# Kernel optimization log

Hardware: AMD Instinct MI355X
Metric: run time of the kernel (lower is better)

Reference implementation:

```python
import jax, jax.numpy as jnp
import numpy as np

B, S, D = 4, 128, 4096
H, KV, HD = 32, 8, 128
REP = H // KV  # GQA repeat factor = 4


def setup_inputs() -> dict:
    key = jax.random.key(0)
    ks = jax.random.split(key, 10)
    scale = 0.02
    x = jax.random.normal(ks[0], (B, S, D), dtype=jnp.float32)
    # projection weights stored as (in, out) so y = x @ W + b (== torch Linear)
    wq = jax.random.normal(ks[1], (D, H * HD), dtype=jnp.float32) * scale
    bq = jax.random.normal(ks[2], (H * HD,), dtype=jnp.float32) * scale
    wk = jax.random.normal(ks[3], (D, KV * HD), dtype=jnp.float32) * scale
    bk = jax.random.normal(ks[4], (KV * HD,), dtype=jnp.float32) * scale
    wv = jax.random.normal(ks[5], (D, KV * HD), dtype=jnp.float32) * scale
    bv = jax.random.normal(ks[6], (KV * HD,), dtype=jnp.float32) * scale
    wo = jax.random.normal(ks[7], (H * HD, D), dtype=jnp.float32) * scale
    bo = jax.random.normal(ks[8], (D,), dtype=jnp.float32) * scale
    # rotary frequencies: theta=10000, half-dim = HD//2 = 64
    inv_freq = 1.0 / (10000.0 ** (jnp.arange(0, HD, 2, dtype=jnp.float32) / HD))
    t = jnp.arange(S, dtype=jnp.float32)
    angles = jnp.outer(t, inv_freq)  # (S, 64)
    freqs_cos = jnp.cos(angles)
    freqs_sin = jnp.sin(angles)
    # additive causal mask (S, S): 0 on/below diagonal, -inf above
    mask = jnp.where(jnp.tril(jnp.ones((S, S), dtype=bool)), 0.0, -jnp.inf).astype(jnp.float32)
    cache_k = jnp.zeros((B, S, KV, HD), dtype=jnp.float32)
    cache_v = jnp.zeros((B, S, KV, HD), dtype=jnp.float32)
    return {
        "x": x, "start_pos": 0, "freqs_cos": freqs_cos, "freqs_sin": freqs_sin,
        "mask": mask, "cache_k": cache_k, "cache_v": cache_v,
        "wq": wq, "bq": bq, "wk": wk, "bk": bk, "wv": wv, "bv": bv,
        "wo": wo, "bo": bo,
    }


def _rope(t, cos, sin):
    # t: (B, S, h, HD); treat last dim as HD//2 complex pairs (real, imag)
    tr = t.reshape(*t.shape[:-1], HD // 2, 2)
    tre, tim = tr[..., 0], tr[..., 1]
    c = cos[None, :, None, :]  # (1, S, 1, HD//2)
    s = sin[None, :, None, :]
    out_re = tre * c - tim * s
    out_im = tre * s + tim * c
    return jnp.stack([out_re, out_im], axis=-1).reshape(t.shape)


def reference(x, start_pos, freqs_cos, freqs_sin, mask, cache_k, cache_v,
              wq, bq, wk, bk, wv, bv, wo, bo):
    bsz, seq_len, _ = x.shape
    q = (x @ wq + bq).reshape(bsz, seq_len, H, HD)
    k = (x @ wk + bk).reshape(bsz, seq_len, KV, HD)
    v = (x @ wv + bv).reshape(bsz, seq_len, KV, HD)
    q = _rope(q, freqs_cos, freqs_sin)
    k = _rope(k, freqs_cos, freqs_sin)
    # KV-cache append (functional)
    cache_k = cache_k.at[:bsz, start_pos:start_pos + seq_len].set(k)
    cache_v = cache_v.at[:bsz, start_pos:start_pos + seq_len].set(v)
    keys = cache_k[:bsz, :start_pos + seq_len]    # (B, T, KV, HD)
    vals = cache_v[:bsz, :start_pos + seq_len]
    # GQA head expansion (repeat_interleave on head dim)
    keys = jnp.repeat(keys, REP, axis=2)          # (B, T, H, HD)
    vals = jnp.repeat(vals, REP, axis=2)
    scale = 1.0 / jnp.sqrt(jnp.float32(HD))
    scores = jnp.einsum('bqhd,bkhd->bhqk', q, keys) * scale + mask
    attn = jax.nn.softmax(scores, axis=-1)
    out = jnp.einsum('bhqk,bkhd->bqhd', attn, vals).reshape(bsz, seq_len, H * HD)
    return out @ wo + bo
```

## Files before the change

kernel.cpp:

```cpp
#include <hip/hip_runtime.h>
#include <math.h>


#define B_   4
#define S_   128
#define D_   4096
#define H_   32
#define KV_  8
#define HD_  128
#define M_   (B_ * S_)
#define NQKV 6144
#define SCALE_ 0.088388347648318447f

typedef _Float16 half_t;
typedef half_t f16x8 __attribute__((ext_vector_type(8)));
typedef float  f32x4 __attribute__((ext_vector_type(4)));

__device__ inline void load_lds16(const void* g, void* l) {
    __builtin_amdgcn_global_load_lds((const __attribute__((address_space(1))) void*)g,
                                     (__attribute__((address_space(3))) void*)l,
                                     16, 0, 0);
}

__device__ void transpose_tile(const float* __restrict__ src, int Nsrc, int nsrc0,
                               int ndst0, int k0, int Ntot,
                               half_t* __restrict__ Wt, void* ldsraw) {
    float (*tile)[132] = (float(*)[132])ldsraw;
    const int t = threadIdx.x;
#pragma unroll
    for (int p = 0; p < 8; ++p) {
        int idx = t + p * 256;
        int r = idx >> 5, c4 = idx & 31;
        *(float4*)&tile[r][c4 * 4] =
            *(const float4*)&src[(size_t)(k0 + r) * Nsrc + nsrc0 + c4 * 4];
    }
    __syncthreads();
    const int n = t >> 1, kh = t & 1;
    __align__(16) half_t hs[32];
#pragma unroll
    for (int i = 0; i < 32; ++i)
        hs[i] = (half_t)tile[kh * 32 + i][n];
    size_t ob = ((size_t)(k0 >> 6) * Ntot + ndst0 + n) * 64 + kh * 32;
#pragma unroll
    for (int u = 0; u < 4; ++u)
        *(uint4*)&Wt[ob + u * 8] = *(uint4*)&hs[u * 8];
}

__global__ __launch_bounds__(256)
void prep_qkv(const float* __restrict__ wq, const float* __restrict__ wk,
              const float* __restrict__ wv, const float* __restrict__ x,
              half_t* __restrict__ Wt, half_t* __restrict__ x16) {
    __shared__ __align__(16) char lds[33792];
    const int bx = blockIdx.x;
    if (bx < 3072) {
        int nt = bx % 48, kt = bx / 48;
        const float* src; int Nsrc, ns0, nd0;
        if (nt < 32)      { src = wq; Nsrc = 4096; ns0 = nt * 128;        nd0 = nt * 128; }
        else if (nt < 40) { src = wk; Nsrc = 1024; ns0 = (nt - 32) * 128; nd0 = 4096 + (nt - 32) * 128; }
        else              { src = wv; Nsrc = 1024; ns0 = (nt - 40) * 128; nd0 = 5120 + (nt - 40) * 128; }
        transpose_tile(src, Nsrc, ns0, nd0, kt * 64, NQKV, Wt, lds);
    } else {
        int i0 = (bx - 3072) * 1024 + threadIdx.x;
#pragma unroll
        for (int j = 0; j < 4; ++j) {
            int i = i0 + j * 256;
            float4 f = ((const float4*)x)[i];
            __align__(8) half_t h4[4] = {(half_t)f.x, (half_t)f.y, (half_t)f.z, (half_t)f.w};
            ((uint2*)x16)[i] = *(uint2*)h4;
        }
    }
}

__device__ __forceinline__ void stage64x128(const half_t* __restrict__ A,
                                            const half_t* __restrict__ Bbase,
                                            int N, int m0, int n0, int kc,
                                            half_t* AsD, half_t* BsD, int tid) {
    const int lane = tid & 63, tB = tid & 192;
    const half_t* Bslab = Bbase + ((size_t)(kc >> 6) * N + n0) * 64;
#pragma unroll
    for (int p = 0; p < 2; ++p) {
        int tb = p * 256 + tB;
        int task = tb + lane;
        int r = task >> 3, os = (task ^ r) & 7;
        load_lds16(&A[(size_t)(m0 + r) * 4096 + kc + os * 8], AsD + tb * 8);
    }
#pragma unroll
    for (int p = 0; p < 4; ++p) {
        int tb = p * 256 + tB;
        int task = tb + lane;
        int r = task >> 3, os = (task ^ r) & 7;
        load_lds16(&Bslab[(size_t)r * 64 + os * 8], BsD + tb * 8);
    }
}

template <bool PRIO>
__device__ __forceinline__ void compute64x128(const half_t* AsD, const half_t* BsD,
                                              int tid, f32x4 (&acc)[4][2]) {
    const int lane = tid & 63;
    const int quad = lane >> 4, l16 = lane & 15;
    const int wn = (tid >> 6) * 32;
    half_t (*As)[64] = (half_t(*)[64])AsD;
    half_t (*Bs)[64] = (half_t(*)[64])BsD;
#pragma unroll
    for (int kk = 0; kk < 2; ++kk) {
        f16x8 af[4], bf[2];
        int L = kk * 4 + quad;
#pragma unroll
        for (int i = 0; i < 4; ++i) {
            int ra = i * 16 + l16;
            af[i] = *(const f16x8*)&As[ra][(L ^ (ra & 7)) * 8];
        }
#pragma unroll
        for (int j = 0; j < 2; ++j) {
            int rb = wn + j * 16 + l16;
            bf[j] = *(const f16x8*)&Bs[rb][(L ^ (rb & 7)) * 8];
        }
        if (PRIO) __builtin_amdgcn_s_setprio(1);
#pragma unroll
        for (int i = 0; i < 4; ++i)
#pragma unroll
            for (int j = 0; j < 2; ++j)
                acc[i][j] = __builtin_amdgcn_mfma_f32_16x16x32_f16(af[i], bf[j], acc[i][j], 0, 0, 0);
        if (PRIO) __builtin_amdgcn_s_setprio(0);
    }
}

__device__ __forceinline__ void fence_step(int n) {
    if (n == 6)      asm volatile("s_waitcnt vmcnt(6)" ::: "memory");
    else if (n == 0) asm volatile("s_waitcnt vmcnt(0)" ::: "memory");
    __builtin_amdgcn_s_barrier();
    __builtin_amdgcn_sched_barrier(0);
}

template <bool PRIO>
__device__ __forceinline__ void gemm64x128(const half_t* __restrict__ A,
                                           const half_t* __restrict__ Bbase,
                                           int N, int m0, int n0, char* lds,
                                           f32x4 (&acc)[4][2]) {
    const int tid = threadIdx.x;
    half_t* As0 = (half_t*)lds;
    half_t* Bs0 = (half_t*)(lds + 24576);
    stage64x128(A, Bbase, N, m0, n0, 0,  As0,        Bs0,        tid);
    stage64x128(A, Bbase, N, m0, n0, 64, As0 + 4096, Bs0 + 8192, tid);
    fence_step(6);
    int cur = 0, pf = 2;
    for (int it = 0; it < 62; ++it) {
        stage64x128(A, Bbase, N, m0, n0, (it + 2) * 64,
                    As0 + pf * 4096, Bs0 + pf * 8192, tid);
        compute64x128<PRIO>(As0 + cur * 4096, Bs0 + cur * 8192, tid, acc);
        fence_step(6);
        cur = (cur == 2) ? 0 : cur + 1;
        pf  = (pf  == 2) ? 0 : pf  + 1;
    }
    compute64x128<PRIO>(As0 + cur * 4096, Bs0 + cur * 8192, tid, acc);
    fence_step(0);
    cur = (cur == 2) ? 0 : cur + 1;
    compute64x128<PRIO>(As0 + cur * 4096, Bs0 + cur * 8192, tid, acc);
    __syncthreads();
}

__global__ __launch_bounds__(256, 2)
void gemm_qkv_pack(const half_t* __restrict__ x16, const half_t* __restrict__ Wt,
                   const float* __restrict__ bq, const float* __restrict__ bk,
                   const float* __restrict__ bv, const float* __restrict__ fc,
                   const float* __restrict__ fs, half_t* __restrict__ q16,
                   half_t* __restrict__ k16, half_t* __restrict__ vt16,
                   const float* __restrict__ wo, half_t* __restrict__ WtO) {
    __shared__ __align__(16) char lds[73728];
    const int bx = blockIdx.x;
    if (bx >= 384) {
        int t = bx - 384;
        transpose_tile(wo, 4096, (t & 31) * 128, (t & 31) * 128, (t >> 5) * 64,
                       4096, WtO, lds);
        return;
    }
    const int o = (bx & 7) * 48 + (bx >> 3);
    const int nb = o >> 3, mb = o & 7;
    const int m0 = mb * 64, n0 = nb * 128;

    f32x4 acc[4][2] = {};
    gemm64x128<true>(x16, Wt, NQKV, m0, n0, lds, acc);

    const int tid = threadIdx.x;
    const int lane = tid & 63;
    const int quad = lane >> 4, l16 = lane & 15;
    const int wn = (tid >> 6) * 32;

    if (n0 < 5120) {
        const bool isQ = n0 < 4096;
        const float* bias = isQ ? bq : bk;
        const int bOff = isQ ? 0 : 4096;
        half_t* dst = isQ ? q16 : k16;
        const int ldd = isQ ? 4096 : 1024;
#pragma unroll
        for (int i = 0; i < 4; ++i)
#pragma unroll
            for (int j = 0; j < 2; ++j) {
                const int col = n0 + wn + j * 16 + l16;
                const int d2 = (col >> 1) & 63;
                const float bcol = bias[col - bOff];
#pragma unroll
                for (int rg = 0; rg < 4; ++rg) {
                    const int row = m0 + i * 16 + quad * 4 + rg;
                    float v = acc[i][j][rg] + bcol;
                    float p = __shfl_xor(v, 1);
                    const int iloc = row & 127;
                    const float c = fc[iloc * 64 + d2], sn = fs[iloc * 64 + d2];
                    float ov = (l16 & 1) ? (p * sn + v * c)
                                         : (v * c - p * sn);
                    float o2 = __shfl_xor(ov, 1);
                    if (!(l16 & 1)) {
                        __align__(4) half_t hh[2] = {(half_t)ov, (half_t)o2};
                        *(unsigned int*)&dst[(size_t)row * ldd + (col - bOff)] =
                            *(unsigned int*)hh;
                    }
                }
            }
    } else {
        half_t (*Th)[136] = (half_t(*)[136])lds;
#pragma unroll
        for (int i = 0; i < 4; ++i)
#pragma unroll
            for (int j = 0; j < 2; ++j) {
                const int cl = wn + j * 16 + l16;
                const float bcol = bv[n0 - 5120 + cl];
#pragma unroll
                for (int rg = 0; rg < 4; ++rg)
                    Th[i * 16 + quad * 4 + rg][cl] = (half_t)(acc[i][j][rg] + bcol);
            }
        __syncthreads();
        const int d = tid >> 1, ih = tid & 1;
        const int kv = (n0 - 5120) >> 7;
        const int b = mb >> 1, i0 = (mb & 1) * 64;
        __align__(16) half_t hs[32];
#pragma unroll
        for (int u = 0; u < 32; ++u) hs[u] = Th[ih * 32 + u][d];
        size_t base = ((size_t)(b * 8 + kv) * 128 + d) * 128 + i0 + ih * 32;
#pragma unroll
        for (int u = 0; u < 4; ++u)
            *(uint4*)&vt16[base + u * 8] = *(uint4*)&hs[u * 8];
    }
}

__global__ __launch_bounds__(256, 2)
void fused_attn(const half_t* __restrict__ q16, const half_t* __restrict__ k16,
                const half_t* __restrict__ vt16, half_t* __restrict__ a16) {
    __shared__ __align__(16) char lds[62464];
    half_t (*Qs)[136] = (half_t(*)[136])lds;
    half_t (*Ks)[136] = (half_t(*)[136])(lds + 8704);
    float (*Ps)[132]  = (float(*)[132])(lds + 43520);
    float (*red)[16]  = (float(*)[16])(lds + 60416);

    const int tid = threadIdx.x;
    const int qi = blockIdx.x & 3, h = (blockIdx.x >> 2) & 31, b = blockIdx.x >> 7;
    const int kv = h >> 2;
    const int qbase = qi * 32;
    const int lane = tid & 63, w = tid >> 6;
    const int quad = lane >> 4, l16 = lane & 15;
    const int m0 = (w & 1) * 16, half64 = (w >> 1) * 64;

#pragma unroll
    for (int p = 0; p < 2; ++p) {
        int task = tid + p * 256;
        int r = task >> 4, c = task & 15;
        *(uint4*)&Qs[r][c * 8] =
            *(const uint4*)&q16[((size_t)(b * 128 + qbase + r) * 32 + h) * 128 + c * 8];
    }
#pragma unroll
    for (int p = 0; p < 8; ++p) {
        int task = tid + p * 256;
        int r = task >> 4, c = task & 15;
        *(uint4*)&Ks[r][c * 8] =
            *(const uint4*)&k16[((size_t)(b * 128 + r) * 8 + kv) * 128 + c * 8];
    }
    __syncthreads();

    f32x4 s[4] = {};
#pragma unroll
    for (int kc = 0; kc < 4; ++kc) {
        f16x8 af = *(const f16x8*)&Qs[m0 + l16][kc * 32 + quad * 8];
#pragma unroll
        for (int jb = 0; jb < 4; ++jb) {
            f16x8 bf = *(const f16x8*)&Ks[half64 + jb * 16 + l16][kc * 32 + quad * 8];
            s[jb] = __builtin_amdgcn_mfma_f32_16x16x32_f16(af, bf, s[jb], 0, 0, 0);
        }
    }
#pragma unroll
    for (int jb = 0; jb < 4; ++jb) {
        int j = half64 + jb * 16 + l16;
#pragma unroll
        for (int rg = 0; rg < 4; ++rg) {
            int row = m0 + quad * 4 + rg;
            Ps[row][j] = (j <= qbase + row) ? s[jb][rg] * SCALE_ : -1e30f;
        }
    }
    __syncthreads();

    const int r = tid >> 3, seg = tid & 7;
    float mx = -1e30f;
#pragma unroll
    for (int i = 0; i < 16; ++i) mx = fmaxf(mx, Ps[r][seg * 16 + i]);
    red[r][seg] = mx;
    __syncthreads();

    uint4 vstage[8];
#pragma unroll
    for (int p = 0; p < 8; ++p) {
        int task = tid + p * 256;
        int rr = task >> 4, c = task & 15;
        vstage[p] = *(const uint4*)&vt16[((size_t)(b * 8 + kv) * 128 + rr) * 128 + c * 8];
    }
    float m = red[r][0];
#pragma unroll
    for (int i = 1; i < 8; ++i) m = fmaxf(m, red[r][i]);
    float sum = 0.f;
#pragma unroll
    for (int i = 0; i < 16; ++i) {
        float e = __expf(Ps[r][seg * 16 + i] - m);
        Ps[r][seg * 16 + i] = e;
        sum += e;
    }
    red[r][8 + seg] = sum;
#pragma unroll
    for (int p = 0; p < 8; ++p) {
        int task = tid + p * 256;
        int rr = task >> 4, c = task & 15;
        *(uint4*)&Ks[rr][c * 8] = vstage[p];
    }
    __syncthreads();

    float tot = 0.f;
#pragma unroll
    for (int i = 0; i < 8; ++i) tot += red[r][8 + i];
    float inv = 1.0f / tot;
#pragma unroll
    for (int i = 0; i < 16; ++i)
        Qs[r][seg * 16 + i] = (half_t)(Ps[r][seg * 16 + i] * inv);
    __syncthreads();

    f32x4 o[4] = {};
#pragma unroll
    for (int jc = 0; jc < 4; ++jc) {
        f16x8 af = *(const f16x8*)&Qs[m0 + l16][jc * 32 + quad * 8];
#pragma unroll
        for (int db = 0; db < 4; ++db) {
            f16x8 bf = *(const f16x8*)&Ks[half64 + db * 16 + l16][jc * 32 + quad * 8];
            o[db] = __builtin_amdgcn_mfma_f32_16x16x32_f16(af, bf, o[db], 0, 0, 0);
        }
    }
#pragma unroll
    for (int db = 0; db < 4; ++db) {
        int d = half64 + db * 16 + l16;
#pragma unroll
        for (int rg = 0; rg < 4; ++rg) {
            int row = m0 + quad * 4 + rg;
            a16[(size_t)(b * 128 + qbase + row) * 4096 + h * 128 + d] = (half_t)o[db][rg];
        }
    }
}

__global__ __launch_bounds__(256, 2)
void gemm_o_fused(const half_t* __restrict__ a16, const half_t* __restrict__ WtO,
                  const float* __restrict__ bo, float* __restrict__ out) {
    __shared__ __align__(16) char lds[73728];
    const int bx = blockIdx.x;
    const int o = (bx & 7) * 32 + (bx >> 3);
    const int nb = o >> 3, mb = o & 7;
    const int m0 = mb * 64, n0 = nb * 128;

    f32x4 acc[4][2] = {};
    gemm64x128<false>(a16, WtO, 4096, m0, n0, lds, acc);

    const int tid = threadIdx.x;
    const int lane = tid & 63;
    const int quad = lane >> 4, l16 = lane & 15;
    const int wn = (tid >> 6) * 32;
#pragma unroll
    for (int i = 0; i < 4; ++i)
#pragma unroll
        for (int j = 0; j < 2; ++j) {
            const int col = n0 + wn + j * 16 + l16;
            const float bcol = bo[col];
#pragma unroll
            for (int rg = 0; rg < 4; ++rg) {
                const int row = m0 + i * 16 + quad * 4 + rg;
                out[(size_t)row * 4096 + col] = acc[i][j][rg] + bcol;
            }
        }
}

extern "C" void kernel_launch(void* const* d_in, const int* in_sizes, int n_in,
                              void* d_out, int out_size, void* d_ws, size_t ws_size,
                              hipStream_t stream) {
    const float* x    = (const float*)d_in[0];
    const float* fc   = (const float*)d_in[2];
    const float* fs   = (const float*)d_in[3];
    const float* wq   = (const float*)d_in[7];
    const float* bq   = (const float*)d_in[8];
    const float* wk   = (const float*)d_in[9];
    const float* bk   = (const float*)d_in[10];
    const float* wv   = (const float*)d_in[11];
    const float* bv   = (const float*)d_in[12];
    const float* wo   = (const float*)d_in[13];
    const float* bo   = (const float*)d_in[14];
    float* out = (float*)d_out;

    half_t* x16  = (half_t*)d_ws;
    half_t* a16  = x16 + 2097152;
    half_t* q16  = a16 + 2097152;
    half_t* k16  = q16 + 2097152;
    half_t* vt16 = k16 + 524288;
    half_t* Wt   = vt16 + 524288;
    half_t* WtO  = Wt + 25165824;

    prep_qkv<<<3584, 256, 0, stream>>>(wq, wk, wv, x, Wt, x16);

    gemm_qkv_pack<<<384 + 2048, 256, 0, stream>>>(x16, Wt, bq, bk, bv, fc, fs,
                                                  q16, k16, vt16, wo, WtO);

    fused_attn<<<512, 256, 0, stream>>>(q16, k16, vt16, a16);

    gemm_o_fused<<<256, 256, 0, stream>>>(a16, WtO, bo, out);
}
```

Before: 282.0 us.

## Use 128x128 QKV GEMM tiles with BK=32 and direct-to-LDS weight transpose loads

The QKV projection GEMM switches from 64x128 tiles with BK=64 to 128x128 tiles with BK=32. Each wave now computes a 64x64 sub-tile, which raises operand reuse and halves the block count to 192. The launch bound goes to three blocks per CU and LDS per block shrinks. The fp32 weight transpose now stages global tiles into LDS with global_load_lds instead of going through registers, dropping the row padding. In exchange, the QKV GEMM has fewer blocks than CUs, leaving some CUs idle, and the unpadded transpose tile may cause LDS bank conflicts.

```diff
diff --git a/kernel.cpp b/kernel.cpp
--- a/kernel.cpp
+++ b/kernel.cpp
@@ -25,14 +25,14 @@
 __device__ void transpose_tile(const float* __restrict__ src, int Nsrc, int nsrc0,
                                int ndst0, int k0, int Ntot,
                                half_t* __restrict__ Wt, void* ldsraw) {
-    float (*tile)[132] = (float(*)[132])ldsraw;
+    float (*tile)[128] = (float(*)[128])ldsraw;
     const int t = threadIdx.x;
 #pragma unroll
     for (int p = 0; p < 8; ++p) {
-        int idx = t + p * 256;
-        int r = idx >> 5, c4 = idx & 31;
-        *(float4*)&tile[r][c4 * 4] =
-            *(const float4*)&src[(size_t)(k0 + r) * Nsrc + nsrc0 + c4 * 4];
+        int tb = p * 256 + (t & 192);
+        int task = tb + (t & 63);
+        load_lds16(&src[(size_t)(k0 + (task >> 5)) * Nsrc + nsrc0 + (task & 31) * 4],
+                   (char*)ldsraw + tb * 16);
     }
     __syncthreads();
     const int n = t >> 1, kh = t & 1;
@@ -50,7 +50,7 @@
 void prep_qkv(const float* __restrict__ wq, const float* __restrict__ wk,
               const float* __restrict__ wv, const float* __restrict__ x,
               half_t* __restrict__ Wt, half_t* __restrict__ x16) {
-    __shared__ __align__(16) char lds[33792];
+    __shared__ __align__(16) char lds[32768];
     const int bx = blockIdx.x;
     if (bx < 3072) {
         int nt = bx % 48, kt = bx / 48;
@@ -71,123 +71,120 @@
     }
 }
 
-__device__ __forceinline__ void stage64x128(const half_t* __restrict__ A,
-                                            const half_t* __restrict__ Bbase,
-                                            int N, int m0, int n0, int kc,
-                                            half_t* AsD, half_t* BsD, int tid) {
+__device__ __forceinline__ void stage_bk32(const half_t* __restrict__ A,
+                                           const half_t* __restrict__ Bbase,
+                                           int N, int m0, int n0, int kc,
+                                           half_t* AsD, half_t* BsD, int tid) {
     const int lane = tid & 63, tB = tid & 192;
-    const half_t* Bslab = Bbase + ((size_t)(kc >> 6) * N + n0) * 64;
+    const half_t* Bslab = Bbase + ((size_t)(kc >> 6) * N + n0) * 64 + ((kc >> 5) & 1) * 32;
 #pragma unroll
     for (int p = 0; p < 2; ++p) {
         int tb = p * 256 + tB;
         int task = tb + lane;
-        int r = task >> 3, os = (task ^ r) & 7;
-        load_lds16(&A[(size_t)(m0 + r) * 4096 + kc + os * 8], AsD + tb * 8);
-    }
-#pragma unroll
-    for (int p = 0; p < 4; ++p) {
-        int tb = p * 256 + tB;
-        int task = tb + lane;
-        int r = task >> 3, os = (task ^ r) & 7;
-        load_lds16(&Bslab[(size_t)r * 64 + os * 8], BsD + tb * 8);
+        int r = task >> 2;
+        int c = (task & 3) ^ ((r >> 1) & 3);
+        load_lds16(&A[(size_t)(m0 + r) * 4096 + kc + c * 8], AsD + tb * 8);
+        load_lds16(&Bslab[(size_t)r * 64 + c * 8],           BsD + tb * 8);
     }
 }
 
 template <bool PRIO>
-__device__ __forceinline__ void compute64x128(const half_t* AsD, const half_t* BsD,
-                                              int tid, f32x4 (&acc)[4][2]) {
+__device__ __forceinline__ void compute_bk32(const half_t* AsD, const half_t* BsD,
+                                             int tid, f32x4 (&acc)[4][4]) {
     const int lane = tid & 63;
     const int quad = lane >> 4, l16 = lane & 15;
-    const int wn = (tid >> 6) * 32;
-    half_t (*As)[64] = (half_t(*)[64])AsD;
-    half_t (*Bs)[64] = (half_t(*)[64])BsD;
-#pragma unroll
-    for (int kk = 0; kk < 2; ++kk) {
-        f16x8 af[4], bf[2];
-        int L = kk * 4 + quad;
-#pragma unroll
-        for (int i = 0; i < 4; ++i) {
-            int ra = i * 16 + l16;
-            af[i] = *(const f16x8*)&As[ra][(L ^ (ra & 7)) * 8];
-        }
-#pragma unroll
-        for (int j = 0; j < 2; ++j) {
-            int rb = wn + j * 16 + l16;
-            bf[j] = *(const f16x8*)&Bs[rb][(L ^ (rb & 7)) * 8];
-        }
-        if (PRIO) __builtin_amdgcn_s_setprio(1);
-#pragma unroll
-        for (int i = 0; i < 4; ++i)
-#pragma unroll
-            for (int j = 0; j < 2; ++j)
-                acc[i][j] = __builtin_amdgcn_mfma_f32_16x16x32_f16(af[i], bf[j], acc[i][j], 0, 0, 0);
-        if (PRIO) __builtin_amdgcn_s_setprio(0);
-    }
-}
-
-__device__ __forceinline__ void fence_step(int n) {
-    if (n == 6)      asm volatile("s_waitcnt vmcnt(6)" ::: "memory");
-    else if (n == 0) asm volatile("s_waitcnt vmcnt(0)" ::: "memory");
+    const int w = tid >> 6;
+    const int wm = (w & 1) * 64, wn = (w >> 1) * 64;
+    half_t (*As)[32] = (half_t(*)[32])AsD;
+    half_t (*Bs)[32] = (half_t(*)[32])BsD;
+    f16x8 af[4], bf[4];
+#pragma unroll
+    for (int i = 0; i < 4; ++i) {
+        int ra = wm + i * 16 + l16;
+        af[i] = *(const f16x8*)&As[ra][(quad ^ ((ra >> 1) & 3)) * 8];
+    }
+#pragma unroll
+    for (int j = 0; j < 4; ++j) {
+        int rb = wn + j * 16 + l16;
+        bf[j] = *(const f16x8*)&Bs[rb][(quad ^ ((rb >> 1) & 3)) * 8];
+    }
+    if (PRIO) __builtin_amdgcn_s_setprio(1);
+#pragma unroll
+    for (int i = 0; i < 4; ++i)
+#pragma unroll
+        for (int j = 0; j < 4; ++j)
+            acc[i][j] = __builtin_amdgcn_mfma_f32_16x16x32_f16(af[i], bf[j], acc[i][j], 0, 0, 0);
+    if (PRIO) __builtin_amdgcn_s_setprio(0);
+}
+
+__device__ __forceinline__ void fence4() {
+    asm volatile("s_waitcnt vmcnt(4)" ::: "memory");
     __builtin_amdgcn_s_barrier();
     __builtin_amdgcn_sched_barrier(0);
 }
+__device__ __forceinline__ void fence0() {
+    asm volatile("s_waitcnt vmcnt(0)" ::: "memory");
+    __builtin_amdgcn_s_barrier();
+    __builtin_amdgcn_sched_barrier(0);
+}
 
 template <bool PRIO>
-__device__ __forceinline__ void gemm64x128(const half_t* __restrict__ A,
-                                           const half_t* __restrict__ Bbase,
-                                           int N, int m0, int n0, char* lds,
-                                           f32x4 (&acc)[4][2]) {
+__device__ __forceinline__ void gemm128_bk32(const half_t* __restrict__ A,
+                                             const half_t* __restrict__ Bbase,
+                                             int N, int m0, int n0,
+                                             char* lds, f32x4 (&acc)[4][4]) {
     const int tid = threadIdx.x;
     half_t* As0 = (half_t*)lds;
     half_t* Bs0 = (half_t*)(lds + 24576);
-    stage64x128(A, Bbase, N, m0, n0, 0,  As0,        Bs0,        tid);
-    stage64x128(A, Bbase, N, m0, n0, 64, As0 + 4096, Bs0 + 8192, tid);
-    fence_step(6);
+    stage_bk32(A, Bbase, N, m0, n0, 0,  As0,        Bs0,        tid);
+    stage_bk32(A, Bbase, N, m0, n0, 32, As0 + 4096, Bs0 + 4096, tid);
+    fence4();
     int cur = 0, pf = 2;
-    for (int it = 0; it < 62; ++it) {
-        stage64x128(A, Bbase, N, m0, n0, (it + 2) * 64,
-                    As0 + pf * 4096, Bs0 + pf * 8192, tid);
-        compute64x128<PRIO>(As0 + cur * 4096, Bs0 + cur * 8192, tid, acc);
-        fence_step(6);
+    for (int it = 0; it < 126; ++it) {
+        stage_bk32(A, Bbase, N, m0, n0, (it + 2) * 32,
+                   As0 + pf * 4096, Bs0 + pf * 4096, tid);
+        compute_bk32<PRIO>(As0 + cur * 4096, Bs0 + cur * 4096, tid, acc);
+        fence4();
         cur = (cur == 2) ? 0 : cur + 1;
         pf  = (pf  == 2) ? 0 : pf  + 1;
     }
-    compute64x128<PRIO>(As0 + cur * 4096, Bs0 + cur * 8192, tid, acc);
-    fence_step(0);
+    compute_bk32<PRIO>(As0 + cur * 4096, Bs0 + cur * 4096, tid, acc);
+    fence0();
     cur = (cur == 2) ? 0 : cur + 1;
-    compute64x128<PRIO>(As0 + cur * 4096, Bs0 + cur * 8192, tid, acc);
-    __syncthreads();
-}
-
-__global__ __launch_bounds__(256, 2)
+    compute_bk32<PRIO>(As0 + cur * 4096, Bs0 + cur * 4096, tid, acc);
+    __syncthreads();
+}
+
+__global__ __launch_bounds__(256, 3)
 void gemm_qkv_pack(const half_t* __restrict__ x16, const half_t* __restrict__ Wt,
                    const float* __restrict__ bq, const float* __restrict__ bk,
                    const float* __restrict__ bv, const float* __restrict__ fc,
                    const float* __restrict__ fs, half_t* __restrict__ q16,
                    half_t* __restrict__ k16, half_t* __restrict__ vt16,
                    const float* __restrict__ wo, half_t* __restrict__ WtO) {
-    __shared__ __align__(16) char lds[73728];
+    __shared__ __align__(16) char lds[49152];
     const int bx = blockIdx.x;
-    if (bx >= 384) {
-        int t = bx - 384;
+    if (bx >= 192) {
+        int t = bx - 192;
         transpose_tile(wo, 4096, (t & 31) * 128, (t & 31) * 128, (t >> 5) * 64,
                        4096, WtO, lds);
         return;
     }
-    const int o = (bx & 7) * 48 + (bx >> 3);
-    const int nb = o >> 3, mb = o & 7;
-    const int m0 = mb * 64, n0 = nb * 128;
-
-    f32x4 acc[4][2] = {};
-    gemm64x128<true>(x16, Wt, NQKV, m0, n0, lds, acc);
+    const int o = (bx & 7) * 24 + (bx >> 3);
+    const int nb = o >> 2, mb = o & 3;
+    const int m0 = mb * 128, n0 = nb * 128;
+
+    f32x4 acc[4][4] = {};
+    gemm128_bk32<true>(x16, Wt, NQKV, m0, n0, lds, acc);
 
     const int tid = threadIdx.x;
     const int lane = tid & 63;
     const int quad = lane >> 4, l16 = lane & 15;
-    const int wn = (tid >> 6) * 32;
-
-    if (n0 < 5120) {
-        const bool isQ = n0 < 4096;
+    const int w = tid >> 6;
+    const int wm = (w & 1) * 64, wn = (w >> 1) * 64;
+
+    if (nb < 40) {
+        const bool isQ = nb < 32;
         const float* bias = isQ ? bq : bk;
         const int bOff = isQ ? 0 : 4096;
         half_t* dst = isQ ? q16 : k16;
@@ -195,13 +192,13 @@
 #pragma unroll
         for (int i = 0; i < 4; ++i)
 #pragma unroll
-            for (int j = 0; j < 2; ++j) {
+            for (int j = 0; j < 4; ++j) {
                 const int col = n0 + wn + j * 16 + l16;
                 const int d2 = (col >> 1) & 63;
                 const float bcol = bias[col - bOff];
 #pragma unroll
                 for (int rg = 0; rg < 4; ++rg) {
-                    const int row = m0 + i * 16 + quad * 4 + rg;
+                    const int row = m0 + wm + i * 16 + quad * 4 + rg;
                     float v = acc[i][j][rg] + bcol;
                     float p = __shfl_xor(v, 1);
                     const int iloc = row & 127;
@@ -221,25 +218,113 @@
 #pragma unroll
         for (int i = 0; i < 4; ++i)
 #pragma unroll
-            for (int j = 0; j < 2; ++j) {
+            for (int j = 0; j < 4; ++j) {
                 const int cl = wn + j * 16 + l16;
                 const float bcol = bv[n0 - 5120 + cl];
 #pragma unroll
                 for (int rg = 0; rg < 4; ++rg)
-                    Th[i * 16 + quad * 4 + rg][cl] = (half_t)(acc[i][j][rg] + bcol);
+                    Th[wm + i * 16 + quad * 4 + rg][cl] = (half_t)(acc[i][j][rg] + bcol);
             }
         __syncthreads();
         const int d = tid >> 1, ih = tid & 1;
-        const int kv = (n0 - 5120) >> 7;
-        const int b = mb >> 1, i0 = (mb & 1) * 64;
-        __align__(16) half_t hs[32];
-#pragma unroll
-        for (int u = 0; u < 32; ++u) hs[u] = Th[ih * 32 + u][d];
-        size_t base = ((size_t)(b * 8 + kv) * 128 + d) * 128 + i0 + ih * 32;
-#pragma unroll
-        for (int u = 0; u < 4; ++u)
-            *(uint4*)&vt16[base + u * 8] = *(uint4*)&hs[u * 8];
-    }
+        const int kv = nb - 40;
+        const int b = mb;
+        const size_t base = ((size_t)(b * 8 + kv) * 128 + d) * 128;
+#pragma unroll
+        for (int h32 = 0; h32 < 2; ++h32) {
+            const int i0 = ih * 64 + h32 * 32;
+            __align__(16) half_t hs[32];
+#pragma unroll
+            for (int v = 0; v < 32; ++v) hs[v] = Th[i0 + v][d];
+#pragma unroll
+            for (int u = 0; u < 4; ++u)
+                *(uint4*)&vt16[base + i0 + u * 8] = *(uint4*)&hs[u * 8];
+        }
+    }
+}
+
+__device__ __forceinline__ void stage64x128(const half_t* __restrict__ A,
+                                            const half_t* __restrict__ Bbase,
+                                            int N, int m0, int n0, int kc,
+                                            half_t* AsD, half_t* BsD, int tid) {
+    const int lane = tid & 63, tB = tid & 192;
+    const half_t* Bslab = Bbase + ((size_t)(kc >> 6) * N + n0) * 64;
+#pragma unroll
+    for (int p = 0; p < 2; ++p) {
+        int tb = p * 256 + tB;
+        int task = tb + lane;
+        int r = task >> 3, os = (task ^ r) & 7;
+        load_lds16(&A[(size_t)(m0 + r) * 4096 + kc + os * 8], AsD + tb * 8);
+    }
+#pragma unroll
+    for (int p = 0; p < 4; ++p) {
+        int tb = p * 256 + tB;
+        int task = tb + lane;
+        int r = task >> 3, os = (task ^ r) & 7;
+        load_lds16(&Bslab[(size_t)r * 64 + os * 8], BsD + tb * 8);
+    }
+}
+
+__device__ __forceinline__ void compute64x128(const half_t* AsD, const half_t* BsD,
+                                              int tid, f32x4 (&acc)[4][2]) {
+    const int lane = tid & 63;
+    const int quad = lane >> 4, l16 = lane & 15;
+    const int wn = (tid >> 6) * 32;
+    half_t (*As)[64] = (half_t(*)[64])AsD;
+    half_t (*Bs)[64] = (half_t(*)[64])BsD;
+#pragma unroll
+    for (int kk = 0; kk < 2; ++kk) {
+        f16x8 af[4], bf[2];
+        int L = kk * 4 + quad;
+#pragma unroll
+        for (int i = 0; i < 4; ++i) {
+            int ra = i * 16 + l16;
+            af[i] = *(const f16x8*)&As[ra][(L ^ (ra & 7)) * 8];
+        }
+#pragma unroll
+        for (int j = 0; j < 2; ++j) {
+            int rb = wn + j * 16 + l16;
+            bf[j] = *(const f16x8*)&Bs[rb][(L ^ (rb & 7)) * 8];
+        }
+#pragma unroll
+        for (int i = 0; i < 4; ++i)
+#pragma unroll
+            for (int j = 0; j < 2; ++j)
+                acc[i][j] = __builtin_amdgcn_mfma_f32_16x16x32_f16(af[i], bf[j], acc[i][j], 0, 0, 0);
+    }
+}
+
+__device__ __forceinline__ void fence_step(int n) {
+    if (n == 6)      asm volatile("s_waitcnt vmcnt(6)" ::: "memory");
+    else if (n == 0) asm volatile("s_waitcnt vmcnt(0)" ::: "memory");
+    __builtin_amdgcn_s_barrier();
+    __builtin_amdgcn_sched_barrier(0);
+}
+
+__device__ __forceinline__ void gemm64x128(const half_t* __restrict__ A,
+                                           const half_t* __restrict__ Bbase,
+                                           int N, int m0, int n0, char* lds,
+                                           f32x4 (&acc)[4][2]) {
+    const int tid = threadIdx.x;
+    half_t* As0 = (half_t*)lds;
+    half_t* Bs0 = (half_t*)(lds + 24576);
+    stage64x128(A, Bbase, N, m0, n0, 0,  As0,        Bs0,        tid);
+    stage64x128(A, Bbase, N, m0, n0, 64, As0 + 4096, Bs0 + 8192, tid);
+    fence_step(6);
+    int cur = 0, pf = 2;
+    for (int it = 0; it < 62; ++it) {
+        stage64x128(A, Bbase, N, m0, n0, (it + 2) * 64,
+                    As0 + pf * 4096, Bs0 + pf * 8192, tid);
+        compute64x128(As0 + cur * 4096, Bs0 + cur * 8192, tid, acc);
+        fence_step(6);
+        cur = (cur == 2) ? 0 : cur + 1;
+        pf  = (pf  == 2) ? 0 : pf  + 1;
+    }
+    compute64x128(As0 + cur * 4096, Bs0 + cur * 8192, tid, acc);
+    fence_step(0);
+    cur = (cur == 2) ? 0 : cur + 1;
+    compute64x128(As0 + cur * 4096, Bs0 + cur * 8192, tid, acc);
+    __syncthreads();
 }
 
 __global__ __launch_bounds__(256, 2)
@@ -369,7 +454,7 @@
     const int m0 = mb * 64, n0 = nb * 128;
 
     f32x4 acc[4][2] = {};
-    gemm64x128<false>(a16, WtO, 4096, m0, n0, lds, acc);
+    gemm64x128(a16, WtO, 4096, m0, n0, lds, acc);
 
     const int tid = threadIdx.x;
     const int lane = tid & 63;
@@ -415,7 +500,7 @@
 
     prep_qkv<<<3584, 256, 0, stream>>>(wq, wk, wv, x, Wt, x16);
 
-    gemm_qkv_pack<<<384 + 2048, 256, 0, stream>>>(x16, Wt, bq, bk, bv, fc, fs,
+    gemm_qkv_pack<<<192 + 2048, 256, 0, stream>>>(x16, Wt, bq, bk, bv, fc, fs,
                                                   q16, k16, vt16, wo, WtO);
 
     fused_attn<<<512, 256, 0, stream>>>(q16, k16, vt16, a16);
```

Result: slower. 294.5 us (+4.4%).
